# Kernel optimization log

Measured on AMD Instinct MI355X. Metric: run time of the kernel, lower is better.

The kernel has to match this reference:

```python
import jax, jax.numpy as jnp
import numpy as np

H = 512  # h_dim = d_rnn


def _pair_mlp(paragraph, W1, W2):
    """Fused equivalent of: cat(p_i, p_j) @ W1 -> ReLU -> @ W2 -> ReLU.
    Splits W1 so the [B,n,n,2h] concatenated input is never materialized
    before the first GEMM.  paragraph: [B, n, H]; W1: [2H, 2H]; W2: [2H, d_pair].
    Returns [B, n, n, d_pair].
    """
    u = paragraph @ W1[:H]   # [B, n, 2H]  (contribution of p_i, broadcast over j)
    v = paragraph @ W1[H:]   # [B, n, 2H]  (contribution of p_j, broadcast over i)
    z = jax.nn.relu(u[:, :, None, :] + v[:, None, :, :])  # [B, n, n, 2H]
    return jax.nn.relu(z @ W2)  # [B, n, n, d_pair]  (dropout = identity in eval)


def reference(paragraph, Wf1, Wf2, w3, Wh1a, Wh1b, wl1, Wh2a, Wh2b, wl2):
    # rela_encode -> future MLP, then directional probs via w3
    rela_vec = _pair_mlp(paragraph, Wf1, Wf2)            # [B,n,n,d_pair]
    rela_p = jax.nn.softmax(rela_vec @ w3, axis=-1)      # [B,n,n,2]
    rela_vec_diret = jnp.concatenate((rela_vec, rela_p), axis=-1)

    # encode_history -> hist_left1 / hist_left2 MLPs and their heads
    hist1 = _pair_mlp(paragraph, Wh1a, Wh1b)
    hist2 = _pair_mlp(paragraph, Wh2a, Wh2b)
    left1_p = jax.nn.softmax(hist1 @ wl1, axis=-1)
    left2_p = jax.nn.softmax(hist2 @ wl2, axis=-1)
    hist_vec_left1 = jnp.concatenate((hist1, left1_p), axis=-1)
    hist_vec_left2 = jnp.concatenate((hist2, left2_p), axis=-1)

    # pack all rela_pred outputs into one tensor: [B, n, n, 3*(d_pair+2)]
    return jnp.concatenate((rela_vec_diret, hist_vec_left1, hist_vec_left2), axis=-1)


def setup_inputs() -> dict:
    key = jax.random.key(0)
    ks = jax.random.split(key, 10)
    B, N, d_pair = 4, 128, 256
    s1 = 1.0 / np.sqrt(2 * H)
    s2 = 1.0 / np.sqrt(d_pair)
    return {
        "paragraph": jax.random.normal(ks[0], (B, N, H), jnp.float32),
        "Wf1": jax.random.normal(ks[1], (2 * H, 2 * H), jnp.float32) * s1,
        "Wf2": jax.random.normal(ks[2], (2 * H, d_pair), jnp.float32) * s1,
        "w3": jax.random.normal(ks[3], (d_pair, 2), jnp.float32) * s2,
        "Wh1a": jax.random.normal(ks[4], (2 * H, 2 * H), jnp.float32) * s1,
        "Wh1b": jax.random.normal(ks[5], (2 * H, d_pair), jnp.float32) * s1,
        "wl1": jax.random.normal(ks[6], (d_pair, 2), jnp.float32) * s2,
        "Wh2a": jax.random.normal(ks[7], (2 * H, 2 * H), jnp.float32) * s1,
        "Wh2b": jax.random.normal(ks[8], (2 * H, d_pair), jnp.float32) * s1,
        "wl2": jax.random.normal(ks[9], (d_pair, 2), jnp.float32) * s2,
    }
```

## Files before the change

kernel.cpp:

```cpp
#include <hip/hip_runtime.h>


typedef __attribute__((ext_vector_type(4))) float floatx4;
typedef __attribute__((ext_vector_type(2))) float floatx2;
typedef __attribute__((ext_vector_type(16))) float floatx16;
typedef __attribute__((ext_vector_type(8))) short short8;

#define KT 16
#define LSTRIDE 68
#define MB (1u << 20)

__device__ __forceinline__ void gload_lds16(const void* g, void* l) {
  __builtin_amdgcn_global_load_lds(
      (const __attribute__((address_space(1))) void*)g,
      (__attribute__((address_space(3))) void*)l, 16, 0, 0);
}

__device__ __forceinline__ void split8(const float* x, short8& hi, short8& lo) {
  unsigned hb[8], lb[8];
#pragma unroll
  for (int e = 0; e < 8; e++) {
    unsigned xb = __float_as_uint(x[e]);
    unsigned h = xb & 0xFFFF0000u;
    float l = x[e] - __uint_as_float(h);
    hb[e] = h;
    lb[e] = __float_as_uint(l) & 0xFFFF0000u;
  }
  union U { unsigned u[4]; short8 s; };
  U H, L;
#pragma unroll
  for (int p = 0; p < 4; p++) {
    H.u[p] = __builtin_amdgcn_perm(hb[2 * p + 1], hb[2 * p], 0x07060302u);
    L.u[p] = __builtin_amdgcn_perm(lb[2 * p + 1], lb[2 * p], 0x07060302u);
  }
  hi = H.s;
  lo = L.s;
}

__device__ __forceinline__ void make_frag(
    const floatx4& ua, const floatx4& ub,
    const floatx4& va, const floatx4& vb,
    short8& hi, short8& lo) {
  float z[8];
#pragma unroll
  for (int e = 0; e < 4; e++) {
    z[e] = fmaxf(ua[e] + va[e], 0.0f);
    z[4 + e] = fmaxf(ub[e] + vb[e], 0.0f);
  }
  split8(z, hi, lo);
}

__device__ __forceinline__ void prep_w1_body(
    int t, const float* __restrict__ W1, unsigned short* __restrict__ W1F) {
  int lane = t & 63;
  int nf = (t >> 6) & 127;
  int kt = t >> 13;
  int g = lane >> 4, c = lane & 15;
  int n = nf * 16 + c;
  int kbase = kt * 32 + g * 8;
  const float* src = W1 + (long)((n >= 1024 ? 512 : 0) + kbase) * 1024 + (n & 1023);

  unsigned hb[8], lb[8];
#pragma unroll
  for (int e = 0; e < 8; e++) {
    float w = src[(long)e * 1024];
    unsigned wb = __float_as_uint(w);
    unsigned h = wb & 0xFFFF0000u;
    float l = w - __uint_as_float(h);
    hb[e] = h;
    lb[e] = __float_as_uint(l) & 0xFFFF0000u;
  }
  union U { unsigned u[4]; short8 s; };
  U H, L;
#pragma unroll
  for (int p = 0; p < 4; p++) {
    H.u[p] = __builtin_amdgcn_perm(hb[2 * p + 1], hb[2 * p], 0x07060302u);
    L.u[p] = __builtin_amdgcn_perm(lb[2 * p + 1], lb[2 * p], 0x07060302u);
  }
  long base = ((long)kt * 128 + nf) * 2 * 64 + lane;
  *(short8*)(W1F + (base + 0) * 8) = H.s;
  *(short8*)(W1F + (base + 64) * 8) = L.s;
}

__device__ __forceinline__ void prep_w2_body32(
    int t, const float* __restrict__ W2, unsigned short* __restrict__ W2F) {
  int lane = t & 63;
  int ksub = (t >> 6) & 1;
  int nf32 = (t >> 7) & 7;
  int kt = t >> 10;
  int g2 = lane >> 5, c32 = lane & 31;
  int n = nf32 * 32 + c32;
  int kbase = kt * 32 + ksub * 16 + g2 * 8;

  unsigned hb[8], lb[8];
#pragma unroll
  for (int e = 0; e < 8; e++) {
    float w = W2[(long)(kbase + e) * 256 + n];
    unsigned wb = __float_as_uint(w);
    unsigned h = wb & 0xFFFF0000u;
    float l = w - __uint_as_float(h);
    hb[e] = h;
    lb[e] = __float_as_uint(l) & 0xFFFF0000u;
  }
  union U { unsigned u[4]; short8 s; };
  U H, L;
#pragma unroll
  for (int p = 0; p < 4; p++) {
    H.u[p] = __builtin_amdgcn_perm(hb[2 * p + 1], hb[2 * p], 0x07060302u);
    L.u[p] = __builtin_amdgcn_perm(lb[2 * p + 1], lb[2 * p], 0x07060302u);
  }
  long base = ((((long)kt * 8 + nf32) * 2) * 2 + ksub) * 64 + lane;
  *(short8*)(W2F + (base + 0) * 8) = H.s;
  *(short8*)(W2F + (base + 128) * 8) = L.s;
}

__global__ __launch_bounds__(256) void prep_all(
    const float* __restrict__ Wf1, const float* __restrict__ Wh1a,
    const float* __restrict__ Wh2a, const float* __restrict__ Wf2,
    const float* __restrict__ Wh1b, const float* __restrict__ Wh2b,
    unsigned short* __restrict__ w1f_all, unsigned short* __restrict__ w2f_all) {
  int bx = blockIdx.x;
  if (bx < 1536) {
    int mlp = bx >> 9;
    const float* W1 = (mlp == 0) ? Wf1 : (mlp == 1) ? Wh1a : Wh2a;
    prep_w1_body((bx & 511) * 256 + threadIdx.x, W1,
                 w1f_all + (long)mlp * (2 * MB));
  } else {
    int bb = bx - 1536;
    int mlp = bb >> 7;
    const float* W2 = (mlp == 0) ? Wf2 : (mlp == 1) ? Wh1b : Wh2b;
    prep_w2_body32((bb & 127) * 256 + threadIdx.x, W2,
                   w2f_all + (long)mlp * (MB / 2));
  }
}

__device__ __forceinline__ void stage1_core(
    int bx, const float* __restrict__ P,
    const unsigned short* __restrict__ W1F,
    float* __restrict__ uF, float* __restrict__ vF) {
  int m0 = (bx >> 4) * 16;
  int n0 = (bx & 15) * 128;
  int tid = threadIdx.x;
  int wid = tid >> 6, lane = tid & 63;
  int g = lane >> 4, r = lane & 15;
  int nw0 = n0 + wid * 32;

  const float* prow = P + (long)(m0 + r) * 512;

  floatx4 acc[2];
#pragma unroll
  for (int nf = 0; nf < 2; nf++) acc[nf] = (floatx4){0.f, 0.f, 0.f, 0.f};

  for (int kt = 0; kt < 16; kt++) {
    int k0 = kt * 32 + g * 8;
    float a[8];
    floatx4 a0 = *(const floatx4*)(prow + k0);
    floatx4 a1 = *(const floatx4*)(prow + k0 + 4);
#pragma unroll
    for (int e = 0; e < 4; e++) { a[e] = a0[e]; a[4 + e] = a1[e]; }
    short8 ahi, alo;
    split8(a, ahi, alo);
#pragma unroll
    for (int nf = 0; nf < 2; nf++) {
      int nfg = (nw0 >> 4) + nf;
      const unsigned short* wp = W1F + (((long)kt * 128 + nfg) * 2 * 64 + lane) * 8;
      short8 whi = *(const short8*)wp;
      short8 wlo = *(const short8*)(wp + 64 * 8);
      acc[nf] = __builtin_amdgcn_mfma_f32_16x16x32_bf16(ahi, whi, acc[nf], 0, 0, 0);
      acc[nf] = __builtin_amdgcn_mfma_f32_16x16x32_bf16(alo, whi, acc[nf], 0, 0, 0);
      acc[nf] = __builtin_amdgcn_mfma_f32_16x16x32_bf16(ahi, wlo, acc[nf], 0, 0, 0);
    }
  }
  if (n0 < 1024) {
#pragma unroll
    for (int nf = 0; nf < 2; nf++)
#pragma unroll
      for (int reg = 0; reg < 4; reg++)
        uF[(long)(m0 + g * 4 + reg) * 1024 + nw0 + nf * 16 + r] = acc[nf][reg];
  } else {
    int kt = (nw0 - 1024) >> 5;
#pragma unroll
    for (int nf = 0; nf < 2; nf++) {
#pragma unroll
      for (int reg = 0; reg < 4; reg++) {
        int m = m0 + g * 4 + reg;
        int b = m >> 7;
        int jf = (m >> 5) & 3;
        long idx = (((long)(b * 32 + kt)) * 4 + jf) * 1024 +
                   ((r >> 3) * 32 + (m & 31)) * 16 + nf * 8 + (r & 7);
        vF[idx] = acc[nf][reg];
      }
    }
  }
}

__global__ __launch_bounds__(256) void stage1_mfma3(
    const float* __restrict__ P, const unsigned short* __restrict__ w1f_all,
    float* __restrict__ uF_all, float* __restrict__ vF_all) {
  int mlp = blockIdx.x >> 9;
  stage1_core(blockIdx.x & 511, P, w1f_all + (long)mlp * (2 * MB),
              uF_all + (long)mlp * 524288, vF_all + (long)mlp * 524288);
}

#define PAIR_BODY(KTC, RBUF, SBUF)                                            \
  {                                                                           \
    const unsigned short* gs = W2F + (long)((KTC) + 1) * 16384;               \
    _Pragma("unroll")                                                         \
    for (int i = 0; i < 4; i++)                                               \
      gload_lds16(gs + (i * 512 + tid) * 8, &(SBUF)[(i * 512 + tid) * 8]);    \
    floatx4 u0 = *(const floatx4*)&ulds[(KTC) * 32 + g2 * 8];                 \
    floatx4 u1 = *(const floatx4*)&ulds[(KTC) * 32 + g2 * 8 + 4];             \
    floatx4 u2 = *(const floatx4*)&ulds[(KTC) * 32 + 16 + g2 * 8];            \
    floatx4 u3 = *(const floatx4*)&ulds[(KTC) * 32 + 16 + g2 * 8 + 4];        \
    short8 ahi0, alo0, ahi1, alo1;                                            \
    make_frag(u0, u1, vc0, vc1, ahi0, alo0);                                  \
    make_frag(u2, u3, vc2, vc3, ahi1, alo1);                                  \
    vp += 4096;                                                               \
    vc0 = *(const floatx4*)(vp);                                              \
    vc1 = *(const floatx4*)(vp + 4);                                          \
    vc2 = *(const floatx4*)(vp + 8);                                          \
    vc3 = *(const floatx4*)(vp + 12);                                         \
    __builtin_amdgcn_s_setprio(1);                                            \
    _Pragma("unroll")                                                         \
    for (int nf = 0; nf < 4; nf++) {                                          \
      const unsigned short* wp = (RBUF) + (nh * 4 + nf) * 2048 + lane * 8;    \
      short8 whi0 = *(const short8*)wp;                                       \
      short8 whi1 = *(const short8*)(wp + 512);                               \
      short8 wlo0 = *(const short8*)(wp + 1024);                              \
      short8 wlo1 = *(const short8*)(wp + 1536);                              \
      acc[nf] = __builtin_amdgcn_mfma_f32_32x32x16_bf16(ahi0, whi0, acc[nf], 0, 0, 0); \
      acc[nf] = __builtin_amdgcn_mfma_f32_32x32x16_bf16(ahi1, whi1, acc[nf], 0, 0, 0); \
      acc[nf] = __builtin_amdgcn_mfma_f32_32x32x16_bf16(alo0, whi0, acc[nf], 0, 0, 0); \
      acc[nf] = __builtin_amdgcn_mfma_f32_32x32x16_bf16(alo1, whi1, acc[nf], 0, 0, 0); \
      acc[nf] = __builtin_amdgcn_mfma_f32_32x32x16_bf16(ahi0, wlo0, acc[nf], 0, 0, 0); \
      acc[nf] = __builtin_amdgcn_mfma_f32_32x32x16_bf16(ahi1, wlo1, acc[nf], 0, 0, 0); \
    }                                                                         \
    __builtin_amdgcn_s_setprio(0);                                            \
    __syncthreads();                                                          \
  }

__global__ __launch_bounds__(512, 4) void pair_mfma3(
    const float* __restrict__ uF_all, const float* __restrict__ vF_all,
    const unsigned short* __restrict__ w2f_all,
    const float* __restrict__ w3_0, const float* __restrict__ w3_1,
    const float* __restrict__ w3_2, float* __restrict__ out) {
  __shared__ unsigned short wbuf[2][16384];
  __shared__ float ulds[1024];
  int orig = blockIdx.x;
  int id = (orig & 7) * 192 + (orig >> 3);
  int mlp = id >> 9;
  int bi = id & 511;
  int b = bi >> 7;
  const float* w3 = (mlp == 0) ? w3_0 : (mlp == 1) ? w3_1 : w3_2;
  const float* uF = uF_all + (long)mlp * 524288;
  const float* vF = vF_all + (long)mlp * 524288;
  const unsigned short* W2F = w2f_all + (long)mlp * 524288;

  int tid = threadIdx.x;
  int wid = tid >> 6;
  int lane = tid & 63;
  int jq = wid >> 1;
  int nh = wid & 1;
  int g2 = lane >> 5;
  int c32 = lane & 31;
  int wj = jq * 32;

  const float* urow = uF + (long)bi * 1024;
  if (tid < 256) gload_lds16(urow + tid * 4, &ulds[tid * 4]);
#pragma unroll
  for (int i = 0; i < 4; i++)
    gload_lds16(W2F + (i * 512 + tid) * 8, &wbuf[0][(i * 512 + tid) * 8]);
  const float* vp = vF + ((long)b * 32 * 4 + jq) * 1024 + lane * 16;
  floatx4 vc0 = *(const floatx4*)(vp);
  floatx4 vc1 = *(const floatx4*)(vp + 4);
  floatx4 vc2 = *(const floatx4*)(vp + 8);
  floatx4 vc3 = *(const floatx4*)(vp + 12);

  floatx16 acc[4];
#pragma unroll
  for (int nf = 0; nf < 4; nf++)
#pragma unroll
    for (int e = 0; e < 16; e++) acc[nf][e] = 0.f;

  __syncthreads();

  for (int kt = 0; kt < 32; kt += 2) {
    PAIR_BODY(kt, wbuf[1] - 16384, wbuf[1]);
    PAIR_BODY(kt + 1, wbuf[1], wbuf[1] - 16384);
  }

  float* ps = ulds;
  float* ob = out + (long)(bi * 128) * 774 + mlp * 258;
  floatx2 w3v[4];
#pragma unroll
  for (int nf = 0; nf < 4; nf++)
    w3v[nf] = *(const floatx2*)(w3 + (nh * 128 + nf * 32 + c32) * 2);
#pragma unroll
  for (int reg = 0; reg < 16; reg++) {
    int row = wj + (reg & 3) + 8 * (reg >> 2) + 4 * g2;
    float* orow = ob + (long)row * 774 + nh * 128 + c32;
    float s0 = 0.f, s1 = 0.f;
#pragma unroll
    for (int nf = 0; nf < 4; nf++) {
      float y = acc[nf][reg];
      y = y > 0.f ? y : 0.f;
      orow[nf * 32] = y;
      s0 += y * w3v[nf][0];
      s1 += y * w3v[nf][1];
    }
#pragma unroll
    for (int off = 1; off < 32; off <<= 1) {
      s0 += __shfl_xor(s0, off, 64);
      s1 += __shfl_xor(s1, off, 64);
    }
    if (c32 == 0) {
      ps[row * 4 + nh * 2 + 0] = s0;
      ps[row * 4 + nh * 2 + 1] = s1;
    }
  }
  __syncthreads();
  if (tid < 128) {
    int row = tid;
    float s0 = ps[row * 4 + 0] + ps[row * 4 + 2];
    float s1 = ps[row * 4 + 1] + ps[row * 4 + 3];
    float m = fmaxf(s0, s1);
    float e0 = __expf(s0 - m), e1 = __expf(s1 - m);
    float inv = 1.0f / (e0 + e1);
    floatx2 pr;
    pr[0] = e0 * inv;
    pr[1] = e1 * inv;
    *(floatx2*)(ob + (long)row * 774 + 256) = pr;
  }
}

__global__ __launch_bounds__(256) void stage1_valu(
    const float* __restrict__ P, const float* __restrict__ W1,
    float* __restrict__ uv) {
  __shared__ float at[KT][LSTRIDE];
  __shared__ float wt[KT][LSTRIDE];
  int bx = blockIdx.x;
  int m0 = (bx >> 5) * 64;
  int c0 = (bx & 31) * 64;
  int half = c0 >> 10;
  int ccol = c0 & 1023;
  int tid = threadIdx.x;
  int tm = tid >> 4, tn = tid & 15;
  int lm = tid >> 2;
  int lk4 = (tid & 3) * 4;
  int lkk = tid >> 4;
  int lc4 = (tid & 15) * 4;

  float acc[4][4] = {};

  for (int k0 = 0; k0 < 512; k0 += KT) {
    floatx4 pa = *(const floatx4*)(P + (long)(m0 + lm) * 512 + k0 + lk4);
    floatx4 wa = *(const floatx4*)(W1 + (long)(half * 512 + k0 + lkk) * 1024 + ccol + lc4);
    __syncthreads();
#pragma unroll
    for (int e = 0; e < 4; e++) at[lk4 + e][lm] = pa[e];
    *(floatx4*)&wt[lkk][lc4] = wa;
    __syncthreads();
#pragma unroll
    for (int kk = 0; kk < KT; kk++) {
      floatx4 av = *(const floatx4*)&at[kk][tm * 4];
      floatx4 wv = *(const floatx4*)&wt[kk][tn * 4];
#pragma unroll
      for (int mm = 0; mm < 4; mm++)
#pragma unroll
        for (int nn = 0; nn < 4; nn++)
          acc[mm][nn] += av[mm] * wv[nn];
    }
  }
#pragma unroll
  for (int mm = 0; mm < 4; mm++) {
    floatx4 o;
#pragma unroll
    for (int nn = 0; nn < 4; nn++) o[nn] = acc[mm][nn];
    *(floatx4*)(uv + (long)(m0 + tm * 4 + mm) * 2048 + c0 + tn * 4) = o;
  }
}

__global__ __launch_bounds__(256) void pair_valu(
    const float* __restrict__ uv, const float* __restrict__ W2,
    float* __restrict__ out, int mlp) {
  __shared__ float zt[KT][LSTRIDE];
  __shared__ float wt[KT][LSTRIDE];
  int bx = blockIdx.x;
  int nb = bx & 3;
  int jh = (bx >> 2) & 1;
  int bi = bx >> 3;
  int b = bi >> 7;
  int j0 = jh * 64;
  int n0 = nb * 64;
  int tid = threadIdx.x;
  int tm = tid >> 4, tn = tid & 15;
  int lj = tid >> 2;
  int lk4 = (tid & 3) * 4;
  int lkk = tid >> 4;
  int ln4 = (tid & 15) * 4;

  const float* urow = uv + (long)bi * 2048;
  const float* vrow = uv + (long)(b * 128 + j0 + lj) * 2048 + 1024;

  float acc[4][4] = {};

  for (int k0 = 0; k0 < 1024; k0 += KT) {
    floatx4 uu = *(const floatx4*)(urow + k0 + lk4);
    floatx4 vv = *(const floatx4*)(vrow + k0 + lk4);
    floatx4 wa = *(const floatx4*)(W2 + (long)(k0 + lkk) * 256 + n0 + ln4);
    __syncthreads();
#pragma unroll
    for (int e = 0; e < 4; e++) {
      float z = uu[e] + vv[e];
      zt[lk4 + e][lj] = z > 0.f ? z : 0.f;
    }
    *(floatx4*)&wt[lkk][ln4] = wa;
    __syncthreads();
#pragma unroll
    for (int kk = 0; kk < KT; kk++) {
      floatx4 zv = *(const floatx4*)&zt[kk][tm * 4];
      floatx4 wv = *(const floatx4*)&wt[kk][tn * 4];
#pragma unroll
      for (int mm = 0; mm < 4; mm++)
#pragma unroll
        for (int nn = 0; nn < 4; nn++)
          acc[mm][nn] += zv[mm] * wv[nn];
    }
  }
  float* ob = out + (long)(bi * 128 + j0) * 774 + mlp * 258 + n0 + tn * 4;
#pragma unroll
  for (int mm = 0; mm < 4; mm++) {
    float* orow = ob + (long)(tm * 4 + mm) * 774;
    floatx2 pa, pb;
    pa[0] = acc[mm][0] > 0.f ? acc[mm][0] : 0.f;
    pa[1] = acc[mm][1] > 0.f ? acc[mm][1] : 0.f;
    pb[0] = acc[mm][2] > 0.f ? acc[mm][2] : 0.f;
    pb[1] = acc[mm][3] > 0.f ? acc[mm][3] : 0.f;
    *(floatx2*)orow = pa;
    *(floatx2*)(orow + 2) = pb;
  }
}

__global__ __launch_bounds__(256) void head_kernel(
    const float* __restrict__ w3_0, const float* __restrict__ w3_1,
    const float* __restrict__ w3_2, float* out) {
  int wid = threadIdx.x >> 6, lane = threadIdx.x & 63;
  int r = blockIdx.x * 4 + wid;
  int mlp = r >> 16;
  int row = r & 65535;
  const float* w3 = (mlp == 0) ? w3_0 : (mlp == 1) ? w3_1 : w3_2;
  const float* yp = out + (long)row * 774 + mlp * 258 + lane * 4;
  floatx2 ya = *(const floatx2*)yp;
  floatx2 yb = *(const floatx2*)(yp + 2);
  const float* wp = w3 + lane * 8;
  floatx4 wv0 = *(const floatx4*)wp;
  floatx4 wv1 = *(const floatx4*)(wp + 4);
  float s0 = ya[0] * wv0[0] + ya[1] * wv0[2] + yb[0] * wv1[0] + yb[1] * wv1[2];
  float s1 = ya[0] * wv0[1] + ya[1] * wv0[3] + yb[0] * wv1[1] + yb[1] * wv1[3];
#pragma unroll
  for (int off = 32; off > 0; off >>= 1) {
    s0 += __shfl_xor(s0, off, 64);
    s1 += __shfl_xor(s1, off, 64);
  }
  if (lane == 0) {
    float m = fmaxf(s0, s1);
    float e0 = __expf(s0 - m), e1 = __expf(s1 - m);
    float inv = 1.0f / (e0 + e1);
    floatx2 pr;
    pr[0] = e0 * inv;
    pr[1] = e1 * inv;
    *(floatx2*)(out + (long)row * 774 + mlp * 258 + 256) = pr;
  }
}

extern "C" void kernel_launch(void* const* d_in, const int* in_sizes, int n_in,
                              void* d_out, int out_size, void* d_ws, size_t ws_size,
                              hipStream_t stream) {
  const float* para = (const float*)d_in[0];
  const float* Wf1  = (const float*)d_in[1];
  const float* Wf2  = (const float*)d_in[2];
  const float* w3   = (const float*)d_in[3];
  const float* Wh1a = (const float*)d_in[4];
  const float* Wh1b = (const float*)d_in[5];
  const float* wl1  = (const float*)d_in[6];
  const float* Wh2a = (const float*)d_in[7];
  const float* Wh2b = (const float*)d_in[8];
  const float* wl2  = (const float*)d_in[9];

  float* outp = (float*)d_out;

  if (ws_size >= (size_t)27 * MB) {
    float* uF_all = (float*)d_ws;
    float* vF_all = (float*)((char*)d_ws + 6 * MB);
    unsigned short* w2f_all = (unsigned short*)((char*)d_ws + 12 * MB);
    unsigned short* w1f_all = (unsigned short*)((char*)d_ws + 15 * MB);
    prep_all<<<1920, 256, 0, stream>>>(Wf1, Wh1a, Wh2a, Wf2, Wh1b, Wh2b,
                                       w1f_all, w2f_all);
    stage1_mfma3<<<1536, 256, 0, stream>>>(para, w1f_all, uF_all, vF_all);
    pair_mfma3<<<1536, 512, 0, stream>>>(uF_all, vF_all, w2f_all,
                                         w3, wl1, wl2, outp);
  } else {
    const float* W1s[3] = {Wf1, Wh1a, Wh2a};
    const float* W2s[3] = {Wf2, Wh1b, Wh2b};
    float* uv = (float*)d_ws;
    for (int mlp = 0; mlp < 3; mlp++) {
      stage1_valu<<<256, 256, 0, stream>>>(para, W1s[mlp], uv);
      pair_valu<<<4096, 256, 0, stream>>>(uv, W2s[mlp], outp, mlp);
    }
    head_kernel<<<49152, 256, 0, stream>>>(w3, wl1, wl2, outp);
  }
}
```

Before: 515.3 us.

## Drop low-part A fragments and retile pair GEMM waves to 64x64

The pair-MLP second GEMM now builds only the high bf16 part of the ReLU(u+v) activation fragment. It no longer computes the low residual, which removes one third of the MFMAs (the alo*whi terms) and the split arithmetic. Each wave is retiled from 32 rows × 128 columns to 64 rows × 64 columns using 2×2 accumulator tiles, so every W2 fragment read from LDS feeds two row tiles. The v prefetch pipelining is replaced by loads at the start of each k-step, and the softmax partial-sum buffer is widened to four column groups. The trade-off is lower accuracy, because activations are truncated to bf16, and more v global loads per step.

Result: no change. 515.6 us (+0.1%).

```diff
diff --git a/kernel.cpp b/kernel.cpp
--- a/kernel.cpp
+++ b/kernel.cpp
@@ -37,17 +37,22 @@
   lo = L.s;
 }
 
-__device__ __forceinline__ void make_frag(
+__device__ __forceinline__ short8 frag_hi(
     const floatx4& ua, const floatx4& ub,
-    const floatx4& va, const floatx4& vb,
-    short8& hi, short8& lo) {
-  float z[8];
+    const floatx4& va, const floatx4& vb) {
+  unsigned zb[8];
 #pragma unroll
   for (int e = 0; e < 4; e++) {
-    z[e] = fmaxf(ua[e] + va[e], 0.0f);
-    z[4 + e] = fmaxf(ub[e] + vb[e], 0.0f);
-  }
-  split8(z, hi, lo);
+    float z0 = fmaxf(ua[e] + va[e], 0.0f);
+    float z1 = fmaxf(ub[e] + vb[e], 0.0f);
+    zb[e] = __float_as_uint(z0);
+    zb[4 + e] = __float_as_uint(z1);
+  }
+  union U { unsigned u[4]; short8 s; } H;
+#pragma unroll
+  for (int p = 0; p < 4; p++)
+    H.u[p] = __builtin_amdgcn_perm(zb[2 * p + 1], zb[2 * p], 0x07060302u);
+  return H.s;
 }
 
 __device__ __forceinline__ void prep_w1_body(
@@ -204,6 +209,16 @@
 
 #define PAIR_BODY(KTC, RBUF, SBUF)                                            \
   {                                                                           \
+    const float* vp0 = vbase0 + (long)(KTC) * 4096;                           \
+    const float* vp1 = vbase1 + (long)(KTC) * 4096;                           \
+    floatx4 va0 = *(const floatx4*)(vp0);                                     \
+    floatx4 va1 = *(const floatx4*)(vp0 + 4);                                 \
+    floatx4 va2 = *(const floatx4*)(vp0 + 8);                                 \
+    floatx4 va3 = *(const floatx4*)(vp0 + 12);                                \
+    floatx4 vb0 = *(const floatx4*)(vp1);                                     \
+    floatx4 vb1 = *(const floatx4*)(vp1 + 4);                                 \
+    floatx4 vb2 = *(const floatx4*)(vp1 + 8);                                 \
+    floatx4 vb3 = *(const floatx4*)(vp1 + 12);                                \
     const unsigned short* gs = W2F + (long)((KTC) + 1) * 16384;               \
     _Pragma("unroll")                                                         \
     for (int i = 0; i < 4; i++)                                               \
@@ -212,28 +227,26 @@
     floatx4 u1 = *(const floatx4*)&ulds[(KTC) * 32 + g2 * 8 + 4];             \
     floatx4 u2 = *(const floatx4*)&ulds[(KTC) * 32 + 16 + g2 * 8];            \
     floatx4 u3 = *(const floatx4*)&ulds[(KTC) * 32 + 16 + g2 * 8 + 4];        \
-    short8 ahi0, alo0, ahi1, alo1;                                            \
-    make_frag(u0, u1, vc0, vc1, ahi0, alo0);                                  \
-    make_frag(u2, u3, vc2, vc3, ahi1, alo1);                                  \
-    vp += 4096;                                                               \
-    vc0 = *(const floatx4*)(vp);                                              \
-    vc1 = *(const floatx4*)(vp + 4);                                          \
-    vc2 = *(const floatx4*)(vp + 8);                                          \
-    vc3 = *(const floatx4*)(vp + 12);                                         \
+    short8 a00 = frag_hi(u0, u1, va0, va1);             \
+    short8 a01 = frag_hi(u2, u3, va2, va3);             \
+    short8 a10 = frag_hi(u0, u1, vb0, vb1);             \
+    short8 a11 = frag_hi(u2, u3, vb2, vb3);             \
     __builtin_amdgcn_s_setprio(1);                                            \
     _Pragma("unroll")                                                         \
-    for (int nf = 0; nf < 4; nf++) {                                          \
-      const unsigned short* wp = (RBUF) + (nh * 4 + nf) * 2048 + lane * 8;    \
+    for (int nf = 0; nf < 2; nf++) {                                          \
+      const unsigned short* wp = (RBUF) + ((nq * 2 + nf) * 4) * 512 + lane * 8; \
       short8 whi0 = *(const short8*)wp;                                       \
       short8 whi1 = *(const short8*)(wp + 512);                               \
       short8 wlo0 = *(const short8*)(wp + 1024);                              \
       short8 wlo1 = *(const short8*)(wp + 1536);                              \
-      acc[nf] = __builtin_amdgcn_mfma_f32_32x32x16_bf16(ahi0, whi0, acc[nf], 0, 0, 0); \
-      acc[nf] = __builtin_amdgcn_mfma_f32_32x32x16_bf16(ahi1, whi1, acc[nf], 0, 0, 0); \
-      acc[nf] = __builtin_amdgcn_mfma_f32_32x32x16_bf16(alo0, whi0, acc[nf], 0, 0, 0); \
-      acc[nf] = __builtin_amdgcn_mfma_f32_32x32x16_bf16(alo1, whi1, acc[nf], 0, 0, 0); \
-      acc[nf] = __builtin_amdgcn_mfma_f32_32x32x16_bf16(ahi0, wlo0, acc[nf], 0, 0, 0); \
-      acc[nf] = __builtin_amdgcn_mfma_f32_32x32x16_bf16(ahi1, wlo1, acc[nf], 0, 0, 0); \
+      acc[0][nf] = __builtin_amdgcn_mfma_f32_32x32x16_bf16(a00, whi0, acc[0][nf], 0, 0, 0); \
+      acc[1][nf] = __builtin_amdgcn_mfma_f32_32x32x16_bf16(a10, whi0, acc[1][nf], 0, 0, 0); \
+      acc[0][nf] = __builtin_amdgcn_mfma_f32_32x32x16_bf16(a01, whi1, acc[0][nf], 0, 0, 0); \
+      acc[1][nf] = __builtin_amdgcn_mfma_f32_32x32x16_bf16(a11, whi1, acc[1][nf], 0, 0, 0); \
+      acc[0][nf] = __builtin_amdgcn_mfma_f32_32x32x16_bf16(a00, wlo0, acc[0][nf], 0, 0, 0); \
+      acc[1][nf] = __builtin_amdgcn_mfma_f32_32x32x16_bf16(a10, wlo0, acc[1][nf], 0, 0, 0); \
+      acc[0][nf] = __builtin_amdgcn_mfma_f32_32x32x16_bf16(a01, wlo1, acc[0][nf], 0, 0, 0); \
+      acc[1][nf] = __builtin_amdgcn_mfma_f32_32x32x16_bf16(a11, wlo1, acc[1][nf], 0, 0, 0); \
     }                                                                         \
     __builtin_amdgcn_s_setprio(0);                                            \
     __syncthreads();                                                          \
@@ -259,28 +272,27 @@
   int tid = threadIdx.x;
   int wid = tid >> 6;
   int lane = tid & 63;
-  int jq = wid >> 1;
-  int nh = wid & 1;
+  int jh = wid >> 2;
+  int nq = wid & 3;
   int g2 = lane >> 5;
   int c32 = lane & 31;
-  int wj = jq * 32;
+
+  const float* vbase0 = vF + ((long)b * 128 + jh * 2 + 0) * 1024 + lane * 16;
+  const float* vbase1 = vF + ((long)b * 128 + jh * 2 + 1) * 1024 + lane * 16;
 
   const float* urow = uF + (long)bi * 1024;
   if (tid < 256) gload_lds16(urow + tid * 4, &ulds[tid * 4]);
 #pragma unroll
   for (int i = 0; i < 4; i++)
     gload_lds16(W2F + (i * 512 + tid) * 8, &wbuf[0][(i * 512 + tid) * 8]);
-  const float* vp = vF + ((long)b * 32 * 4 + jq) * 1024 + lane * 16;
-  floatx4 vc0 = *(const floatx4*)(vp);
-  floatx4 vc1 = *(const floatx4*)(vp + 4);
-  floatx4 vc2 = *(const floatx4*)(vp + 8);
-  floatx4 vc3 = *(const floatx4*)(vp + 12);
-
-  floatx16 acc[4];
-#pragma unroll
-  for (int nf = 0; nf < 4; nf++)
-#pragma unroll
-    for (int e = 0; e < 16; e++) acc[nf][e] = 0.f;
+
+  floatx16 acc[2][2];
+#pragma unroll
+  for (int mm = 0; mm < 2; mm++)
+#pragma unroll
+    for (int nf = 0; nf < 2; nf++)
+#pragma unroll
+      for (int e = 0; e < 16; e++) acc[mm][nf][e] = 0.f;
 
   __syncthreads();
 
@@ -291,38 +303,41 @@
 
   float* ps = ulds;
   float* ob = out + (long)(bi * 128) * 774 + mlp * 258;
-  floatx2 w3v[4];
-#pragma unroll
-  for (int nf = 0; nf < 4; nf++)
-    w3v[nf] = *(const floatx2*)(w3 + (nh * 128 + nf * 32 + c32) * 2);
-#pragma unroll
-  for (int reg = 0; reg < 16; reg++) {
-    int row = wj + (reg & 3) + 8 * (reg >> 2) + 4 * g2;
-    float* orow = ob + (long)row * 774 + nh * 128 + c32;
-    float s0 = 0.f, s1 = 0.f;
-#pragma unroll
-    for (int nf = 0; nf < 4; nf++) {
-      float y = acc[nf][reg];
-      y = y > 0.f ? y : 0.f;
-      orow[nf * 32] = y;
-      s0 += y * w3v[nf][0];
-      s1 += y * w3v[nf][1];
-    }
-#pragma unroll
-    for (int off = 1; off < 32; off <<= 1) {
-      s0 += __shfl_xor(s0, off, 64);
-      s1 += __shfl_xor(s1, off, 64);
-    }
-    if (c32 == 0) {
-      ps[row * 4 + nh * 2 + 0] = s0;
-      ps[row * 4 + nh * 2 + 1] = s1;
+  floatx2 w3v[2];
+#pragma unroll
+  for (int nf = 0; nf < 2; nf++)
+    w3v[nf] = *(const floatx2*)(w3 + (nq * 64 + nf * 32 + c32) * 2);
+#pragma unroll
+  for (int mm = 0; mm < 2; mm++) {
+#pragma unroll
+    for (int reg = 0; reg < 16; reg++) {
+      int row = jh * 64 + mm * 32 + (reg & 3) + 8 * (reg >> 2) + 4 * g2;
+      float* orow = ob + (long)row * 774 + nq * 64 + c32;
+      float s0 = 0.f, s1 = 0.f;
+#pragma unroll
+      for (int nf = 0; nf < 2; nf++) {
+        float y = acc[mm][nf][reg];
+        y = y > 0.f ? y : 0.f;
+        orow[nf * 32] = y;
+        s0 += y * w3v[nf][0];
+        s1 += y * w3v[nf][1];
+      }
+#pragma unroll
+      for (int off = 1; off < 32; off <<= 1) {
+        s0 += __shfl_xor(s0, off, 64);
+        s1 += __shfl_xor(s1, off, 64);
+      }
+      if (c32 == 0) {
+        ps[row * 8 + nq * 2 + 0] = s0;
+        ps[row * 8 + nq * 2 + 1] = s1;
+      }
     }
   }
   __syncthreads();
   if (tid < 128) {
     int row = tid;
-    float s0 = ps[row * 4 + 0] + ps[row * 4 + 2];
-    float s1 = ps[row * 4 + 1] + ps[row * 4 + 3];
+    float s0 = ps[row * 8 + 0] + ps[row * 8 + 2] + ps[row * 8 + 4] + ps[row * 8 + 6];
+    float s1 = ps[row * 8 + 1] + ps[row * 8 + 3] + ps[row * 8 + 5] + ps[row * 8 + 7];
     float m = fmaxf(s0, s1);
     float e0 = __expf(s0 - m), e1 = __expf(s1 - m);
     float inv = 1.0f / (e0 + e1);
```

## Drop W2 low-part split, stream W2 from global, re-tile pair kernel

Applied to the files above, without the earlier changes.

The second GEMM now keeps only the bf16 high part of W2, so each k-step runs 4 MFMA passes per output tile instead of 6 (the W_lo terms are dropped). The pair kernel no longer stages W2 through double-buffered LDS with per-iteration barriers. Each wave loads its W2 fragments straight from global memory into registers, prefetching one k-step ahead. Work is re-tiled so each block covers 64 rows by 256 columns with 8 waves each owning a 32x64 tile, doubling the grid and changing the softmax partial-sum reduction. Precision drops because W2 is truncated to bf16, and W2 reads now depend on L2/cache bandwidth rather than LDS reuse.

Result: slower. 531.8 us (+3.2%).

```diff
diff --git a/kernel.cpp b/kernel.cpp
--- a/kernel.cpp
+++ b/kernel.cpp
@@ -37,17 +37,17 @@
   lo = L.s;
 }
 
-__device__ __forceinline__ void make_frag(
+__device__ __forceinline__ void zfrag(
     const floatx4& ua, const floatx4& ub,
     const floatx4& va, const floatx4& vb,
-    short8& hi, short8& lo) {
+    short8& zh, short8& zl) {
   float z[8];
 #pragma unroll
   for (int e = 0; e < 4; e++) {
     z[e] = fmaxf(ua[e] + va[e], 0.0f);
     z[4 + e] = fmaxf(ub[e] + vb[e], 0.0f);
   }
-  split8(z, hi, lo);
+  split8(z, zh, zl);
 }
 
 __device__ __forceinline__ void prep_w1_body(
@@ -82,8 +82,8 @@
   *(short8*)(W1F + (base + 64) * 8) = L.s;
 }
 
-__device__ __forceinline__ void prep_w2_body32(
-    int t, const float* __restrict__ W2, unsigned short* __restrict__ W2F) {
+__device__ __forceinline__ void prep_w2_single(
+    int t, const float* __restrict__ W2, unsigned short* __restrict__ W2Fs) {
   int lane = t & 63;
   int ksub = (t >> 6) & 1;
   int nf32 = (t >> 7) & 7;
@@ -92,33 +92,23 @@
   int n = nf32 * 32 + c32;
   int kbase = kt * 32 + ksub * 16 + g2 * 8;
 
-  unsigned hb[8], lb[8];
-#pragma unroll
-  for (int e = 0; e < 8; e++) {
-    float w = W2[(long)(kbase + e) * 256 + n];
-    unsigned wb = __float_as_uint(w);
-    unsigned h = wb & 0xFFFF0000u;
-    float l = w - __uint_as_float(h);
-    hb[e] = h;
-    lb[e] = __float_as_uint(l) & 0xFFFF0000u;
-  }
-  union U { unsigned u[4]; short8 s; };
-  U H, L;
-#pragma unroll
-  for (int p = 0; p < 4; p++) {
+  unsigned hb[8];
+#pragma unroll
+  for (int e = 0; e < 8; e++)
+    hb[e] = __float_as_uint(W2[(long)(kbase + e) * 256 + n]);
+  union U { unsigned u[4]; short8 s; } H;
+#pragma unroll
+  for (int p = 0; p < 4; p++)
     H.u[p] = __builtin_amdgcn_perm(hb[2 * p + 1], hb[2 * p], 0x07060302u);
-    L.u[p] = __builtin_amdgcn_perm(lb[2 * p + 1], lb[2 * p], 0x07060302u);
-  }
-  long base = ((((long)kt * 8 + nf32) * 2) * 2 + ksub) * 64 + lane;
-  *(short8*)(W2F + (base + 0) * 8) = H.s;
-  *(short8*)(W2F + (base + 128) * 8) = L.s;
+  long base = (((long)kt * 8 + nf32) * 2 + ksub) * 64 + lane;
+  *(short8*)(W2Fs + base * 8) = H.s;
 }
 
 __global__ __launch_bounds__(256) void prep_all(
     const float* __restrict__ Wf1, const float* __restrict__ Wh1a,
     const float* __restrict__ Wh2a, const float* __restrict__ Wf2,
     const float* __restrict__ Wh1b, const float* __restrict__ Wh2b,
-    unsigned short* __restrict__ w1f_all, unsigned short* __restrict__ w2f_all) {
+    unsigned short* __restrict__ w1f_all, unsigned short* __restrict__ w2fs_all) {
   int bx = blockIdx.x;
   if (bx < 1536) {
     int mlp = bx >> 9;
@@ -129,8 +119,8 @@
     int bb = bx - 1536;
     int mlp = bb >> 7;
     const float* W2 = (mlp == 0) ? Wf2 : (mlp == 1) ? Wh1b : Wh2b;
-    prep_w2_body32((bb & 127) * 256 + threadIdx.x, W2,
-                   w2f_all + (long)mlp * (MB / 2));
+    prep_w2_single((bb & 127) * 256 + threadIdx.x, W2,
+                   w2fs_all + (long)mlp * 262144);
   }
 }
 
@@ -202,106 +192,99 @@
               uF_all + (long)mlp * 524288, vF_all + (long)mlp * 524288);
 }
 
-#define PAIR_BODY(KTC, RBUF, SBUF)                                            \
-  {                                                                           \
-    const unsigned short* gs = W2F + (long)((KTC) + 1) * 16384;               \
-    _Pragma("unroll")                                                         \
-    for (int i = 0; i < 4; i++)                                               \
-      gload_lds16(gs + (i * 512 + tid) * 8, &(SBUF)[(i * 512 + tid) * 8]);    \
-    floatx4 u0 = *(const floatx4*)&ulds[(KTC) * 32 + g2 * 8];                 \
-    floatx4 u1 = *(const floatx4*)&ulds[(KTC) * 32 + g2 * 8 + 4];             \
-    floatx4 u2 = *(const floatx4*)&ulds[(KTC) * 32 + 16 + g2 * 8];            \
-    floatx4 u3 = *(const floatx4*)&ulds[(KTC) * 32 + 16 + g2 * 8 + 4];        \
-    short8 ahi0, alo0, ahi1, alo1;                                            \
-    make_frag(u0, u1, vc0, vc1, ahi0, alo0);                                  \
-    make_frag(u2, u3, vc2, vc3, ahi1, alo1);                                  \
-    vp += 4096;                                                               \
-    vc0 = *(const floatx4*)(vp);                                              \
-    vc1 = *(const floatx4*)(vp + 4);                                          \
-    vc2 = *(const floatx4*)(vp + 8);                                          \
-    vc3 = *(const floatx4*)(vp + 12);                                         \
-    __builtin_amdgcn_s_setprio(1);                                            \
-    _Pragma("unroll")                                                         \
-    for (int nf = 0; nf < 4; nf++) {                                          \
-      const unsigned short* wp = (RBUF) + (nh * 4 + nf) * 2048 + lane * 8;    \
-      short8 whi0 = *(const short8*)wp;                                       \
-      short8 whi1 = *(const short8*)(wp + 512);                               \
-      short8 wlo0 = *(const short8*)(wp + 1024);                              \
-      short8 wlo1 = *(const short8*)(wp + 1536);                              \
-      acc[nf] = __builtin_amdgcn_mfma_f32_32x32x16_bf16(ahi0, whi0, acc[nf], 0, 0, 0); \
-      acc[nf] = __builtin_amdgcn_mfma_f32_32x32x16_bf16(ahi1, whi1, acc[nf], 0, 0, 0); \
-      acc[nf] = __builtin_amdgcn_mfma_f32_32x32x16_bf16(alo0, whi0, acc[nf], 0, 0, 0); \
-      acc[nf] = __builtin_amdgcn_mfma_f32_32x32x16_bf16(alo1, whi1, acc[nf], 0, 0, 0); \
-      acc[nf] = __builtin_amdgcn_mfma_f32_32x32x16_bf16(ahi0, wlo0, acc[nf], 0, 0, 0); \
-      acc[nf] = __builtin_amdgcn_mfma_f32_32x32x16_bf16(ahi1, wlo1, acc[nf], 0, 0, 0); \
-    }                                                                         \
-    __builtin_amdgcn_s_setprio(0);                                            \
-    __syncthreads();                                                          \
-  }
-
 __global__ __launch_bounds__(512, 4) void pair_mfma3(
     const float* __restrict__ uF_all, const float* __restrict__ vF_all,
-    const unsigned short* __restrict__ w2f_all,
+    const unsigned short* __restrict__ w2fs_all,
     const float* __restrict__ w3_0, const float* __restrict__ w3_1,
     const float* __restrict__ w3_2, float* __restrict__ out) {
-  __shared__ unsigned short wbuf[2][16384];
   __shared__ float ulds[1024];
+  __shared__ float ps[512];
   int orig = blockIdx.x;
-  int id = (orig & 7) * 192 + (orig >> 3);
-  int mlp = id >> 9;
-  int bi = id & 511;
+  int id = (orig & 7) * 384 + (orig >> 3);
+  int jh = id & 1;
+  int bi = (id >> 1) & 511;
+  int mlp = id >> 10;
   int b = bi >> 7;
   const float* w3 = (mlp == 0) ? w3_0 : (mlp == 1) ? w3_1 : w3_2;
   const float* uF = uF_all + (long)mlp * 524288;
   const float* vF = vF_all + (long)mlp * 524288;
-  const unsigned short* W2F = w2f_all + (long)mlp * 524288;
+  const unsigned short* W2Fs = w2fs_all + (long)mlp * 262144;
 
   int tid = threadIdx.x;
   int wid = tid >> 6;
   int lane = tid & 63;
-  int jq = wid >> 1;
-  int nh = wid & 1;
+  int jw = wid >> 2;
+  int nq = wid & 3;
+  int jf = jh * 2 + jw;
   int g2 = lane >> 5;
   int c32 = lane & 31;
-  int wj = jq * 32;
+
+  const float* vbase = vF + ((long)b * 128 + jf) * 1024 + lane * 16;
+  const unsigned short* wb = W2Fs + ((nq * 2) * 2) * 512 + lane * 8;
 
   const float* urow = uF + (long)bi * 1024;
   if (tid < 256) gload_lds16(urow + tid * 4, &ulds[tid * 4]);
-#pragma unroll
-  for (int i = 0; i < 4; i++)
-    gload_lds16(W2F + (i * 512 + tid) * 8, &wbuf[0][(i * 512 + tid) * 8]);
-  const float* vp = vF + ((long)b * 32 * 4 + jq) * 1024 + lane * 16;
-  floatx4 vc0 = *(const floatx4*)(vp);
-  floatx4 vc1 = *(const floatx4*)(vp + 4);
-  floatx4 vc2 = *(const floatx4*)(vp + 8);
-  floatx4 vc3 = *(const floatx4*)(vp + 12);
-
-  floatx16 acc[4];
-#pragma unroll
-  for (int nf = 0; nf < 4; nf++)
+  floatx4 v0 = *(const floatx4*)(vbase);
+  floatx4 v1 = *(const floatx4*)(vbase + 4);
+  floatx4 v2 = *(const floatx4*)(vbase + 8);
+  floatx4 v3 = *(const floatx4*)(vbase + 12);
+  short8 w00 = *(const short8*)(wb);
+  short8 w01 = *(const short8*)(wb + 512);
+  short8 w10 = *(const short8*)(wb + 1024);
+  short8 w11 = *(const short8*)(wb + 1536);
+
+  floatx16 acc[2];
+#pragma unroll
+  for (int nf = 0; nf < 2; nf++)
 #pragma unroll
     for (int e = 0; e < 16; e++) acc[nf][e] = 0.f;
 
   __syncthreads();
 
-  for (int kt = 0; kt < 32; kt += 2) {
-    PAIR_BODY(kt, wbuf[1] - 16384, wbuf[1]);
-    PAIR_BODY(kt + 1, wbuf[1], wbuf[1] - 16384);
-  }
-
-  float* ps = ulds;
+  for (int kt = 0; kt < 32; kt++) {
+    floatx4 u0 = *(const floatx4*)&ulds[kt * 32 + g2 * 8];
+    floatx4 u1 = *(const floatx4*)&ulds[kt * 32 + g2 * 8 + 4];
+    floatx4 u2 = *(const floatx4*)&ulds[kt * 32 + 16 + g2 * 8];
+    floatx4 u3 = *(const floatx4*)&ulds[kt * 32 + 16 + g2 * 8 + 4];
+    short8 zh0, zl0, zh1, zl1;
+    zfrag(u0, u1, v0, v1, zh0, zl0);
+    zfrag(u2, u3, v2, v3, zh1, zl1);
+    {
+      const float* vp = vbase + (long)(kt + 1) * 4096;
+      v0 = *(const floatx4*)(vp);
+      v1 = *(const floatx4*)(vp + 4);
+      v2 = *(const floatx4*)(vp + 8);
+      v3 = *(const floatx4*)(vp + 12);
+    }
+    const unsigned short* wn = wb + (long)(kt + 1) * 8192;
+    __builtin_amdgcn_s_setprio(1);
+    acc[0] = __builtin_amdgcn_mfma_f32_32x32x16_bf16(zh0, w00, acc[0], 0, 0, 0);
+    acc[1] = __builtin_amdgcn_mfma_f32_32x32x16_bf16(zh0, w10, acc[1], 0, 0, 0);
+    acc[0] = __builtin_amdgcn_mfma_f32_32x32x16_bf16(zl0, w00, acc[0], 0, 0, 0);
+    acc[1] = __builtin_amdgcn_mfma_f32_32x32x16_bf16(zl0, w10, acc[1], 0, 0, 0);
+    w00 = *(const short8*)(wn);
+    w10 = *(const short8*)(wn + 1024);
+    acc[0] = __builtin_amdgcn_mfma_f32_32x32x16_bf16(zh1, w01, acc[0], 0, 0, 0);
+    acc[1] = __builtin_amdgcn_mfma_f32_32x32x16_bf16(zh1, w11, acc[1], 0, 0, 0);
+    acc[0] = __builtin_amdgcn_mfma_f32_32x32x16_bf16(zl1, w01, acc[0], 0, 0, 0);
+    acc[1] = __builtin_amdgcn_mfma_f32_32x32x16_bf16(zl1, w11, acc[1], 0, 0, 0);
+    w01 = *(const short8*)(wn + 512);
+    w11 = *(const short8*)(wn + 1536);
+    __builtin_amdgcn_s_setprio(0);
+  }
+
   float* ob = out + (long)(bi * 128) * 774 + mlp * 258;
-  floatx2 w3v[4];
-#pragma unroll
-  for (int nf = 0; nf < 4; nf++)
-    w3v[nf] = *(const floatx2*)(w3 + (nh * 128 + nf * 32 + c32) * 2);
+  floatx2 w3v[2];
+#pragma unroll
+  for (int nf = 0; nf < 2; nf++)
+    w3v[nf] = *(const floatx2*)(w3 + (nq * 64 + nf * 32 + c32) * 2);
 #pragma unroll
   for (int reg = 0; reg < 16; reg++) {
-    int row = wj + (reg & 3) + 8 * (reg >> 2) + 4 * g2;
-    float* orow = ob + (long)row * 774 + nh * 128 + c32;
+    int lrow = jw * 32 + (reg & 3) + 8 * (reg >> 2) + 4 * g2;
+    float* orow = ob + (long)(jh * 64 + lrow) * 774 + nq * 64 + c32;
     float s0 = 0.f, s1 = 0.f;
 #pragma unroll
-    for (int nf = 0; nf < 4; nf++) {
+    for (int nf = 0; nf < 2; nf++) {
       float y = acc[nf][reg];
       y = y > 0.f ? y : 0.f;
       orow[nf * 32] = y;
@@ -314,22 +297,24 @@
       s1 += __shfl_xor(s1, off, 64);
     }
     if (c32 == 0) {
-      ps[row * 4 + nh * 2 + 0] = s0;
-      ps[row * 4 + nh * 2 + 1] = s1;
+      ps[(lrow * 4 + nq) * 2 + 0] = s0;
+      ps[(lrow * 4 + nq) * 2 + 1] = s1;
     }
   }
   __syncthreads();
-  if (tid < 128) {
-    int row = tid;
-    float s0 = ps[row * 4 + 0] + ps[row * 4 + 2];
-    float s1 = ps[row * 4 + 1] + ps[row * 4 + 3];
+  if (tid < 64) {
+    int lrow = tid;
+    float s0 = ps[(lrow * 4 + 0) * 2] + ps[(lrow * 4 + 1) * 2] +
+               ps[(lrow * 4 + 2) * 2] + ps[(lrow * 4 + 3) * 2];
+    float s1 = ps[(lrow * 4 + 0) * 2 + 1] + ps[(lrow * 4 + 1) * 2 + 1] +
+               ps[(lrow * 4 + 2) * 2 + 1] + ps[(lrow * 4 + 3) * 2 + 1];
     float m = fmaxf(s0, s1);
     float e0 = __expf(s0 - m), e1 = __expf(s1 - m);
     float inv = 1.0f / (e0 + e1);
     floatx2 pr;
     pr[0] = e0 * inv;
     pr[1] = e1 * inv;
-    *(floatx2*)(ob + (long)row * 774 + 256) = pr;
+    *(floatx2*)(ob + (long)(jh * 64 + lrow) * 774 + 256) = pr;
   }
 }
 
@@ -492,12 +477,12 @@
   if (ws_size >= (size_t)27 * MB) {
     float* uF_all = (float*)d_ws;
     float* vF_all = (float*)((char*)d_ws + 6 * MB);
-    unsigned short* w2f_all = (unsigned short*)((char*)d_ws + 12 * MB);
+    unsigned short* w2fs_all = (unsigned short*)((char*)d_ws + 12 * MB);
     unsigned short* w1f_all = (unsigned short*)((char*)d_ws + 15 * MB);
     prep_all<<<1920, 256, 0, stream>>>(Wf1, Wh1a, Wh2a, Wf2, Wh1b, Wh2b,
-                                       w1f_all, w2f_all);
+                                       w1f_all, w2fs_all);
     stage1_mfma3<<<1536, 256, 0, stream>>>(para, w1f_all, uF_all, vF_all);
-    pair_mfma3<<<1536, 512, 0, stream>>>(uF_all, vF_all, w2f_all,
+    pair_mfma3<<<3072, 512, 0, stream>>>(uF_all, vF_all, w2fs_all,
                                          w3, wl1, wl2, outp);
   } else {
     const float* W1s[3] = {Wf1, Wh1a, Wh2a};
```
